# Performance work log

Hardware: AMD Instinct MI355X
Metric: run time of the kernel (lower is better)

The kernel has to match this reference:

```python
import jax, jax.numpy as jnp
from jax import lax
import numpy as np

SEQ_LEN = 96; PRED_LEN = 96; SIGNAL_LEN = 16; NUM_NODES = 256
EMBED = 128; HIDDEN = 64; K_NN = 8; S_SCALE = 2.0; CHEB_ORDER = 2
MA_K = 3; BATCH = 16
C_FREQ = SIGNAL_LEN // 2 + 1          # 9 rfft bins
M_NODES = NUM_NODES * C_FREQ          # nodes per sample graph


def _sin_posemb(pos, dim):
    half = dim // 2
    freqs = 1.0 / (10000.0 ** (np.arange(half) / half))
    ang = pos[:, None] * freqs[None, :]
    return np.concatenate([np.sin(ang), np.cos(ang)], axis=-1).astype(np.float32)


def setup_inputs():
    key = jax.random.key(0)
    ks = jax.random.split(key, 12)
    x = jax.random.normal(ks[0], (BATCH, SEQ_LEN, NUM_NODES), jnp.float32)
    # Chebyshev (order 2) approx of Haar framelet filters cos(xi/2), sin(xi/2) on [0, pi]
    t = np.linspace(-1.0, 1.0, 201); xi = (t + 1.0) * np.pi / 2.0
    ch = np.polynomial.chebyshev
    approx = np.stack([ch.chebfit(t, np.cos(xi / 2.0), CHEB_ORDER),
                       ch.chebfit(t, np.sin(xi / 2.0), CHEB_ORDER)]).astype(np.float32)
    freq_emb = _sin_posemb(np.arange(C_FREQ, dtype=np.float32) * S_SCALE, EMBED)
    sc = (2.0 / EMBED) ** 0.5
    return dict(
        x=x,
        approx=jnp.asarray(approx),                 # [F=2, K=3]
        theta=jnp.ones((2,), jnp.float32),
        fr_Wr=jax.random.normal(ks[1], (EMBED, EMBED), jnp.float32) * sc,
        fr_Wi=jax.random.normal(ks[2], (EMBED, EMBED), jnp.float32) * sc,
        eo_Wr=jax.random.normal(ks[3], (1, EMBED), jnp.float32) * sc,
        eo_Wi=jax.random.normal(ks[4], (1, EMBED), jnp.float32) * sc,
        freq_emb=jnp.asarray(freq_emb),             # [C, EMBED]
        n1_w=jnp.ones((NUM_NODES,), jnp.float32), n1_b=jnp.zeros((NUM_NODES,), jnp.float32),
        n2_w=jnp.ones((NUM_NODES,), jnp.float32), n2_b=jnp.zeros((NUM_NODES,), jnp.float32),
        W1_w=jax.random.normal(ks[5], (HIDDEN, SEQ_LEN), jnp.float32) * (1.0 / SEQ_LEN ** 0.5),
        W1_b=jnp.zeros((HIDDEN,), jnp.float32),
        W2_w=jax.random.normal(ks[6], (HIDDEN, HIDDEN), jnp.float32) * (1.0 / HIDDEN ** 0.5),
        W2_b=jnp.zeros((HIDDEN,), jnp.float32),
        Wt_w=jax.random.normal(ks[7], (HIDDEN, SEQ_LEN), jnp.float32) * (1.0 / SEQ_LEN ** 0.5),
        Wt_b=jnp.zeros((HIDDEN,), jnp.float32),
        W3_w=jax.random.normal(ks[8], (PRED_LEN, HIDDEN), jnp.float32) * (1.0 / HIDDEN ** 0.5),
        W3_b=jnp.zeros((PRED_LEN,), jnp.float32),
    )


def _clinear(z, Wr, Wi):
    xr, xi = z.real, z.imag
    return lax.complex(xr @ Wr.T - xi @ Wi.T, xr @ Wi.T + xi @ Wr.T)


def _csilu(z):
    return lax.complex(jax.nn.silu(z.real), jax.nn.silu(z.imag))


def _cheb_prop(h, row, col, ew, coeffs):
    # Chebyshev recurrence with A_norm(h) = scatter_add(row, (ew/s) * h[col])
    w = (ew / S_SCALE)[:, None]
    def A(hh):
        return jnp.zeros_like(hh).at[row].add(w * hh[col])
    Tx0 = h
    out = coeffs[0] * Tx0
    Tx1 = -A(Tx0)
    out = out + coeffs[1] * Tx1
    for ki in range(2, CHEB_ORDER + 1):
        Tx2 = -2.0 * A(Tx1) - Tx0
        out = out + coeffs[ki] * Tx2
        Tx0, Tx1 = Tx1, Tx2
    return out


def _knn_one(feat):
    # feat [M, 2] -> symmetrised degree-normalised KNN edges
    sq = jnp.sum(feat * feat, axis=1)
    d2 = sq[:, None] + sq[None, :] - 2.0 * (feat @ feat.T)
    d2 = jnp.where(jnp.eye(M_NODES, dtype=bool), jnp.inf, d2)
    idx = lax.top_k(-d2, K_NN)[1]                      # smallest distances
    src = jnp.repeat(jnp.arange(M_NODES), K_NN)
    dst = idx.reshape(-1)
    r = jnp.concatenate([src, dst])
    c = jnp.concatenate([dst, src])
    deg = jnp.zeros((M_NODES,), jnp.float32).at[r].add(1.0)
    dinv = (deg + 1e-8) ** -0.5
    return r, c, dinv[r] * dinv[c]


def _moving_avg(x):
    pad = MA_K // 2
    front = jnp.repeat(x[:, :1, :], pad, axis=1)
    back = jnp.repeat(x[:, -1:, :], MA_K - 1 - pad, axis=1)
    xp = jnp.concatenate([front, x, back], axis=1)     # (B, T+k-1, N)
    cs = jnp.cumsum(xp, axis=1)
    cs = jnp.concatenate([jnp.zeros_like(cs[:, :1, :]), cs], axis=1)
    return (cs[:, MA_K:, :] - cs[:, :-MA_K, :]) / MA_K  # (B, T, N)


def _inorm(h, w, b):
    mu = jnp.mean(h, axis=-1, keepdims=True)
    var = jnp.mean((h - mu) ** 2, axis=-1, keepdims=True)
    return (h - mu) / jnp.sqrt(var + 1e-5) * w[None, :, None] + b[None, :, None]


def _forward(x, approx, theta, fr_Wr, fr_Wi, eo_Wr, eo_Wi, freq_emb,
             n1_w, n1_b, n2_w, n2_b, W1_w, W1_b, W2_w, W2_b, Wt_w, Wt_b, W3_w, W3_b):
    B, T, N = x.shape
    trend = _moving_avg(x)
    seasonal = x - trend
    S = jnp.fft.rfft(seasonal, n=SIGNAL_LEN, axis=1, norm='ortho')   # (B, C, N) c64
    S_perm = jnp.transpose(S, (0, 2, 1))                             # (B, N, C)
    node_feat = S_perm[..., None] * freq_emb                         # (B, N, C, E) c64
    batch_x = node_feat.reshape(B * M_NODES, EMBED)
    sg = S_perm.reshape(B, M_NODES)
    feat = lax.stop_gradient(jnp.stack([sg.real, sg.imag], axis=-1))  # (B, M, 2)
    rs, cs_, ews = jax.vmap(_knn_one)(feat)
    off = (jnp.arange(B) * M_NODES)[:, None]
    row = (rs + off).reshape(-1)
    col = (cs_ + off).reshape(-1)
    ew = ews.reshape(-1)
    # framelet layer: sum of F filtered Chebyshev propagations
    acc = jnp.zeros_like(batch_x)
    for i in range(approx.shape[0]):
        acc = acc + theta[i] * _cheb_prop(batch_x, row, col, ew, approx[i])
    h = _csilu(_clinear(acc, fr_Wr, fr_Wi))
    S_out = _clinear(h, eo_Wr, eo_Wi).reshape(B, N, C_FREQ)
    H = jnp.fft.irfft(jnp.transpose(S_out, (0, 2, 1)), n=SEQ_LEN, axis=1, norm='ortho')
    H = jnp.transpose(H, (0, 2, 1))                                  # (B, N, T)
    H = jax.nn.silu(_inorm(H, n1_w, n1_b))
    H = H @ W1_w.T + W1_b
    H = jax.nn.silu(_inorm(H, n2_w, n2_b))
    H = H @ W2_w.T + W2_b
    trend_emb = jnp.transpose(trend, (0, 2, 1)) @ Wt_w.T + Wt_b
    return (H + trend_emb) @ W3_w.T + W3_b                           # (B, N, pred_len)


def reference(x, approx, theta, fr_Wr, fr_Wi, eo_Wr, eo_Wi, freq_emb,
              n1_w, n1_b, n2_w, n2_b, W1_w, W1_b, W2_w, W2_b, Wt_w, Wt_b, W3_w, W3_b):
    return _forward(x, approx, theta, fr_Wr, fr_Wi, eo_Wr, eo_Wi, freq_emb,
                    n1_w, n1_b, n2_w, n2_b, W1_w, W1_b, W2_w, W2_b, Wt_w, Wt_b, W3_w, W3_b)
```

## Files before the change

### kernel.cpp

```cpp
#include <hip/hip_runtime.h>
#include <math.h>
#include <float.h>

#define BATCH 16
#define SEQ 96
#define NNODE 256
#define CFREQ 9
#define MNODE (NNODE * CFREQ)
#define BM (BATCH * MNODE)
#define KNN 8
#define EMBED 128
#define HIDDEN 64
#define TN (SEQ * NNODE)
#define KCAP 64
#define NBLK (BM / 256)
#define HROWS 16
#define FEW (CFREQ * EMBED)

__constant__ float COS16[16] = {
    1.0f, 0.9238795325112867f, 0.7071067811865476f, 0.3826834323650898f,
    0.0f, -0.3826834323650898f, -0.7071067811865476f, -0.9238795325112867f,
    -1.0f, -0.9238795325112867f, -0.7071067811865476f, -0.3826834323650898f,
    0.0f, 0.3826834323650898f, 0.7071067811865476f, 0.9238795325112867f};
__constant__ float SIN16[16] = {
    0.0f, 0.3826834323650898f, 0.7071067811865476f, 0.9238795325112867f,
    1.0f, 0.9238795325112867f, 0.7071067811865476f, 0.3826834323650898f,
    0.0f, -0.3826834323650898f, -0.7071067811865476f, -0.9238795325112867f,
    -1.0f, -0.9238795325112867f, -0.7071067811865476f, -0.3826834323650898f};

static __device__ __forceinline__ float silu_f(float x) {
    return x / (1.0f + expf(-x));
}

static __device__ __forceinline__ float rank_h(float2 fj, float xi2, float yi2) {
    float sqj = __fmaf_rn(fj.y, fj.y, __fmul_rn(fj.x, fj.x));
    return __fmaf_rn(xi2, fj.x, __fmaf_rn(yi2, fj.y, sqj));
}

__global__ void __launch_bounds__(256) prep_kernel(
    const float* __restrict__ x, float* __restrict__ S, int* __restrict__ cnt,
    const float* __restrict__ femb, const float* __restrict__ Wr,
    const float* __restrict__ Wi, float* __restrict__ FE, int* __restrict__ gtotal) {
    int gid = blockIdx.x * 256 + threadIdx.x;
    if (gid < BM) {
        if (gid == 0) *gtotal = 0;
        cnt[gid] = 0;
        int b = gid / MNODE;
        int m = gid - b * MNODE;
        int n = m / CFREQ;
        int c = m - n * CFREQ;
        const float* xb = x + b * TN + n;
        float xv[17];
        #pragma unroll
        for (int t = 0; t < 17; ++t) xv[t] = xb[t * NNODE];
        float re = 0.0f, im = 0.0f;
        #pragma unroll
        for (int t = 0; t < 16; ++t) {
            int tm = t > 0 ? t - 1 : 0;
            float tr = (xv[tm] + xv[t] + xv[t + 1]) * (1.0f / 3.0f);
            float s = xv[t] - tr;
            int k = (c * t) & 15;
            re += s * COS16[k];
            im -= s * SIN16[k];
        }
        S[gid * 2 + 0] = re * 0.25f;
        S[gid * 2 + 1] = im * 0.25f;
    } else {
        int f = gid - BM;
        if (f < FEW) {
            int c = f / EMBED;
            int e = f - c * EMBED;
            float ar = 0.0f, ai = 0.0f;
            for (int k = 0; k < EMBED; ++k) {
                float fv = femb[c * EMBED + k];
                ar += fv * Wr[e * EMBED + k];
                ai += fv * Wi[e * EMBED + k];
            }
            FE[f * 2 + 0] = ar;
            FE[f * 2 + 1] = ai;
        }
    }
}

__global__ void __launch_bounds__(256, 8) knn_kernel(const float* __restrict__ S,
                                                     int* __restrict__ idx, int* __restrict__ cnt) {
    __shared__ float2 f[MNODE];
    __shared__ unsigned long long kbuf[4][KCAP];
    int b = blockIdx.y;
    int tid = threadIdx.x;
    for (int t = tid; t < MNODE; t += 256) {
        f[t] = make_float2(S[(b * MNODE + t) * 2 + 0], S[(b * MNODE + t) * 2 + 1]);
    }
    __syncthreads();
    int wave = tid >> 6, lane = tid & 63;
    int i = blockIdx.x * 4 + wave;
    float2 fi = f[i];
    float xi2 = __fmul_rn(-2.0f, fi.x), yi2 = __fmul_rn(-2.0f, fi.y);
    int lane_i = __builtin_amdgcn_readfirstlane(i & 63);
    int k_i    = __builtin_amdgcn_readfirstlane(i >> 6);

    float h[36];
    float mymin = FLT_MAX;
    #pragma unroll
    for (int k = 0; k < 36; ++k) {
        int j = lane + (k << 6);
        float hh = rank_h(f[j], xi2, yi2);
        if (k == k_i && lane == lane_i) hh = FLT_MAX;
        h[k] = hh;
        mymin = fminf(mymin, hh);
    }
    float g = mymin;
    g = fminf(g, __shfl_xor(g, 1, 64));
    g = fminf(g, __shfl_xor(g, 2, 64));
    g = fminf(g, __shfl_xor(g, 4, 64));
    float T = g;
    T = fmaxf(T, __shfl_xor(T, 8, 64));
    T = fmaxf(T, __shfl_xor(T, 16, 64));
    T = fmaxf(T, __shfl_xor(T, 32, 64));
    unsigned long long* mybuf = kbuf[wave];
    const unsigned long long lmask = (1ull << lane) - 1ull;
    int total = 0;
    #pragma unroll
    for (int k = 0; k < 36; ++k) {
        bool pred = h[k] <= T;
        unsigned long long mask = __ballot(pred);
        if (pred) {
            int pos = total + (int)__popcll(mask & lmask);
            if (pos < KCAP) {
                unsigned int bits = __float_as_uint(h[k]);
                if (bits == 0x80000000u) bits = 0u;
                unsigned int s = bits ^ (unsigned int)(((int)bits >> 31) | 0x80000000);
                mybuf[pos] = ((unsigned long long)s << 32) | (unsigned int)(lane + (k << 6));
            }
        }
        total += (int)__popcll(mask);
    }

    if (total >= KNN && total <= KCAP) {
        int padded = (total + 7) & ~7;
        if (lane < padded - total) mybuf[total + lane] = ~0ull;
        for (int p = lane; p < total; p += 64) {
            unsigned long long mykey = mybuf[p];
            int rank = 0;
            for (int q = 0; q < padded; q += 8) {
                const ulonglong2* bp = (const ulonglong2*)&mybuf[q];
                ulonglong2 a = bp[0], b2 = bp[1], c2 = bp[2], d2 = bp[3];
                rank += (int)(a.x  < mykey) + (int)(a.y  < mykey)
                      + (int)(b2.x < mykey) + (int)(b2.y < mykey)
                      + (int)(c2.x < mykey) + (int)(c2.y < mykey)
                      + (int)(d2.x < mykey) + (int)(d2.y < mykey);
            }
            if (rank < KNN) {
                int j = (int)(unsigned int)(mykey & 0xFFFFFFFFull);
                idx[(b * MNODE + i) * KNN + rank] = j;
                atomicAdd(&cnt[b * MNODE + j], 1);
            }
        }
    } else {
        const unsigned long long SENT = ~0ull;
        unsigned long long k0 = SENT, k1 = SENT, k2 = SENT, k3 = SENT,
                           k4 = SENT, k5 = SENT, k6 = SENT, k7 = SENT;
        #pragma unroll
        for (int k = 0; k < 36; ++k) {
            unsigned int bits = __float_as_uint(h[k]);
            if (bits == 0x80000000u) bits = 0u;
            unsigned int s = bits ^ (unsigned int)(((int)bits >> 31) | 0x80000000);
            unsigned long long key = ((unsigned long long)s << 32) | (unsigned int)(lane + (k << 6));
            if (key < k7) {
                k7 = key;
                if (k7 < k6) { unsigned long long t = k6; k6 = k7; k7 = t; }
                if (k6 < k5) { unsigned long long t = k5; k5 = k6; k6 = t; }
                if (k5 < k4) { unsigned long long t = k4; k4 = k5; k5 = t; }
                if (k4 < k3) { unsigned long long t = k3; k3 = k4; k4 = t; }
                if (k3 < k2) { unsigned long long t = k2; k2 = k3; k3 = t; }
                if (k2 < k1) { unsigned long long t = k1; k1 = k2; k2 = t; }
                if (k1 < k0) { unsigned long long t = k0; k0 = k1; k1 = t; }
            }
        }
        unsigned long long mywin = 0;
        #pragma unroll
        for (int r = 0; r < KNN; ++r) {
            unsigned long long hh = k0;
            #pragma unroll
            for (int off = 32; off > 0; off >>= 1) {
                unsigned long long o = __shfl_xor(hh, off, 64);
                if (o < hh) hh = o;
            }
            if (lane == r) mywin = hh;
            if (k0 == hh) {
                k0 = k1; k1 = k2; k2 = k3; k3 = k4; k4 = k5; k5 = k6; k6 = k7; k7 = SENT;
            }
        }
        if (lane < KNN) {
            int j = (int)(unsigned int)(mywin & 0xFFFFFFFFull);
            idx[(b * MNODE + i) * KNN + lane] = j;
            atomicAdd(&cnt[b * MNODE + j], 1);
        }
    }
}

__global__ void __launch_bounds__(256) scan_kernel(
    const int* __restrict__ cnt, const float* __restrict__ S,
    float* __restrict__ dinv, float* __restrict__ PS,
    int* __restrict__ gtotal, int2* __restrict__ oc, int* __restrict__ fptr) {
    __shared__ int wsum[4];
    __shared__ int sbase;
    int tid = threadIdx.x;
    int lane = tid & 63, wv = tid >> 6;
    int gid = blockIdx.x * 256 + tid;
    int v = cnt[gid];
    float deg = (float)(KNN + v);
    float dv = 1.0f / sqrtf(deg + 1e-8f);
    dinv[gid] = dv;
    PS[gid * 2 + 0] = dv * S[gid * 2 + 0];
    PS[gid * 2 + 1] = dv * S[gid * 2 + 1];
    int x = v;
    #pragma unroll
    for (int off = 1; off < 64; off <<= 1) {
        int y = __shfl_up(x, off, 64);
        if (lane >= off) x += y;
    }
    if (lane == 63) wsum[wv] = x;
    __syncthreads();
    if (tid == 0) sbase = atomicAdd(gtotal, wsum[0] + wsum[1] + wsum[2] + wsum[3]);
    __syncthreads();
    int base = sbase;
    for (int w = 0; w < wv; ++w) base += wsum[w];
    int o = base + x - v;
    oc[gid] = make_int2(o, v);
    fptr[gid] = o;
}

__global__ void fill_kernel(const int* __restrict__ idx,
                            int* __restrict__ fptr, int* __restrict__ rev) {
    int gid = blockIdx.x * blockDim.x + threadIdx.x;
    if (gid >= BM * KNN) return;
    int b = gid / (MNODE * KNN);
    int rem = gid - b * (MNODE * KNN);
    int i = rem / KNN;
    int gj = b * MNODE + idx[gid];
    int pos = atomicAdd(&fptr[gj], 1);
    rev[pos] = b * MNODE + i;
}

__global__ void __launch_bounds__(256) gather1_kernel(
    const int* __restrict__ idx, const int2* __restrict__ oc,
    const int* __restrict__ rev, const float* __restrict__ dinv, const float* __restrict__ PS,
    float* __restrict__ zA, float* __restrict__ zAw) {
    int gid = blockIdx.x * blockDim.x + threadIdx.x;
    if (gid >= BM * CFREQ) return;
    int gi = gid / CFREQ;
    int c = gid - gi * CFREQ;
    int b = gi / MNODE;
    float ax = 0.0f, ay = 0.0f;
    #pragma unroll
    for (int k = 0; k < KNN; ++k) {
        int gj = b * MNODE + idx[gi * KNN + k];
        bool m = (gj % CFREQ) == c;
        float2 p = ((const float2*)PS)[gj];
        ax += m ? p.x : 0.0f;
        ay += m ? p.y : 0.0f;
    }
    int2 ocv = oc[gi];
    int o = ocv.x, e = o + ocv.y;
    for (int p_ = o; p_ < e; ++p_) {
        int gk = rev[p_];
        bool m = (gk % CFREQ) == c;
        float2 p = ((const float2*)PS)[gk];
        ax += m ? p.x : 0.0f;
        ay += m ? p.y : 0.0f;
    }
    float dv = dinv[gi];
    float s = dv * 0.5f;
    float zx = s * ax, zy = s * ay;
    zA[gid * 2 + 0] = zx;
    zA[gid * 2 + 1] = zy;
    zAw[gid * 2 + 0] = dv * zx;
    zAw[gid * 2 + 1] = dv * zy;
}

__global__ void __launch_bounds__(256) g2proj_kernel(
    const int* __restrict__ idx, const int2* __restrict__ oc,
    const int* __restrict__ rev, const float* __restrict__ dinv,
    const float* __restrict__ zA, const float* __restrict__ zAw,
    const float* __restrict__ S, const float* __restrict__ FE,
    const float* __restrict__ eoWr, const float* __restrict__ eoWi,
    const float* __restrict__ theta, const float* __restrict__ approx,
    float* __restrict__ Sout) {
    __shared__ float2 zfb[4][CFREQ];
    int wave = threadIdx.x >> 6;
    int lane = threadIdx.x & 63;
    int r = blockIdx.x * 4 + wave;
    if (r >= BM) return;
    float a0 = theta[0] * approx[0] + theta[1] * approx[3];
    float a1 = theta[0] * approx[1] + theta[1] * approx[4];
    float a2 = theta[0] * approx[2] + theta[1] * approx[5];
    float ca = a0 - a2, cb = -a1, cc = 2.0f * a2;
    int b = r / MNODE;
    int2 ocv = oc[r];
    if (lane < 36) {
        int c = lane >> 2, sub = lane & 3;
        float ax = 0.0f, ay = 0.0f;
        #pragma unroll
        for (int k = sub; k < KNN; k += 4) {
            int gj = b * MNODE + idx[r * KNN + k];
            float2 v = ((const float2*)zAw)[gj * CFREQ + c];
            ax += v.x;
            ay += v.y;
        }
        int o = ocv.x, e = o + ocv.y;
        for (int p = o + sub; p < e; p += 4) {
            int gk = rev[p];
            float2 v = ((const float2*)zAw)[gk * CFREQ + c];
            ax += v.x;
            ay += v.y;
        }
        ax += __shfl_xor(ax, 1, 64);  ay += __shfl_xor(ay, 1, 64);
        ax += __shfl_xor(ax, 2, 64);  ay += __shfl_xor(ay, 2, 64);
        if (sub == 0) {
            float s = dinv[r] * 0.5f;
            float2 za = ((const float2*)zA)[r * CFREQ + c];
            zfb[wave][c] = make_float2(cb * za.x + cc * (s * ax),
                                       cb * za.y + cc * (s * ay));
        }
    }
    int cr = r % CFREQ;
    float sr = S[r * 2 + 0], si = S[r * 2 + 1];
    int e1 = lane + 64;
    float ur0 = 0.0f, ui0 = 0.0f, ur1 = 0.0f, ui1 = 0.0f;
    #pragma unroll
    for (int c = 0; c < CFREQ; ++c) {
        float2 zf = zfb[wave][c];
        float zr = zf.x, zi = zf.y;
        if (c == cr) { zr += ca * sr; zi += ca * si; }
        float fr0 = FE[(c * EMBED + lane) * 2 + 0], fi0 = FE[(c * EMBED + lane) * 2 + 1];
        float fr1 = FE[(c * EMBED + e1) * 2 + 0],  fi1 = FE[(c * EMBED + e1) * 2 + 1];
        ur0 += zr * fr0 - zi * fi0;  ui0 += zr * fi0 + zi * fr0;
        ur1 += zr * fr1 - zi * fi1;  ui1 += zr * fi1 + zi * fr1;
    }
    float hr0 = silu_f(ur0), hi0 = silu_f(ui0);
    float hr1 = silu_f(ur1), hi1 = silu_f(ui1);
    float wr0 = eoWr[lane], wi0 = eoWi[lane], wr1 = eoWr[e1], wi1 = eoWi[e1];
    float p = hr0 * wr0 - hi0 * wi0 + hr1 * wr1 - hi1 * wi1;
    float q = hr0 * wi0 + hi0 * wr0 + hr1 * wi1 + hi1 * wr1;
    #pragma unroll
    for (int off = 32; off > 0; off >>= 1) {
        p += __shfl_down(p, off, 64);
        q += __shfl_down(q, off, 64);
    }
    if (lane == 0) {
        Sout[r * 2 + 0] = p;
        Sout[r * 2 + 1] = q;
    }
}

__global__ void __launch_bounds__(1024) head_kernel(
    const float* __restrict__ Sout, const float* __restrict__ x,
    const float* __restrict__ n1w, const float* __restrict__ n1b,
    const float* __restrict__ n2w, const float* __restrict__ n2b,
    const float* __restrict__ W1w, const float* __restrict__ W1b,
    const float* __restrict__ W2w, const float* __restrict__ W2b,
    const float* __restrict__ Wtw, const float* __restrict__ Wtb,
    const float* __restrict__ W3w, const float* __restrict__ W3b,
    float* __restrict__ out) {
    __shared__ float tabc[96], tabs[96];
    __shared__ float srow[HROWS][18];
    __shared__ float tbuf[HROWS][96];
    __shared__ float hraw[HROWS][96];
    __shared__ float sH[HROWS][96];
    __shared__ float h2[HROWS][64];
    __shared__ float s3[HROWS][64];
    __shared__ float red[HROWS][2];
    __shared__ float wbuf[6240];
    int tid = threadIdx.x;
    int wave = tid >> 6, lane = tid & 63;
    int bn0 = blockIdx.x * HROWS;
    if (tid < 96) {
        double a = 6.283185307179586476925286766559 * (double)tid / 96.0;
        tabc[tid] = (float)cos(a);
        tabs[tid] = (float)sin(a);
    }
    for (int i = tid; i < HROWS * 96; i += 1024) {
        int g = i / 96, t = i - g * 96;
        int bn = bn0 + g;
        hraw[g][t] = x[(bn >> 8) * TN + t * NNODE + (bn & 255)];
    }
    if (tid < HROWS * 18) {
        int g = tid / 18, k = tid - g * 18;
        srow[g][k] = Sout[(bn0 + g) * 18 + k];
    }
    __syncthreads();
    for (int i = tid; i < HROWS * 96; i += 1024) {
        int g = i / 96, t = i - g * 96;
        int tm = t > 0 ? t - 1 : 0;
        int tp = t < SEQ - 1 ? t + 1 : SEQ - 1;
        tbuf[g][t] = (hraw[g][tm] + hraw[g][t] + hraw[g][tp]) * (1.0f / 3.0f);
    }
    __syncthreads();
    for (int i = tid; i < HROWS * 96; i += 1024) {
        int g = i / 96, t = i - g * 96;
        float acc = srow[g][0];
        #pragma unroll
        for (int c = 1; c < CFREQ; ++c) {
            int k = (c * t) % 96;
            acc += 2.0f * (srow[g][2 * c] * tabc[k] - srow[g][2 * c + 1] * tabs[k]);
        }
        hraw[g][t] = acc * 0.10206207261596575f;
    }
    __syncthreads();
    {
        float v = hraw[wave][lane] + ((lane < 32) ? hraw[wave][64 + lane] : 0.0f);
        #pragma unroll
        for (int off = 32; off > 0; off >>= 1) v += __shfl_down(v, off, 64);
        if (lane == 0) red[wave][0] = v * (1.0f / 96.0f);
    }
    __syncthreads();
    {
        float mu = red[wave][0];
        float d0 = hraw[wave][lane] - mu;
        float v = d0 * d0;
        if (lane < 32) { float d1 = hraw[wave][64 + lane] - mu; v += d1 * d1; }
        #pragma unroll
        for (int off = 32; off > 0; off >>= 1) v += __shfl_down(v, off, 64);
        if (lane == 0) red[wave][1] = v * (1.0f / 96.0f);
    }
    __syncthreads();
    for (int i = tid; i < HROWS * 96; i += 1024) {
        int g = i / 96, t = i - g * 96;
        int n = (bn0 + g) & 255;
        float xn = (hraw[g][t] - red[g][0]) / sqrtf(red[g][1] + 1e-5f) * n1w[n] + n1b[n];
        sH[g][t] = silu_f(xn);
    }
    for (int i = tid; i < HIDDEN * 96; i += 1024) {
        int rr = i / 96;
        wbuf[rr * 97 + (i - rr * 96)] = W1w[i];
    }
    __syncthreads();
    float v1;
    {
        float acc = W1b[lane];
        #pragma unroll 8
        for (int t = 0; t < 96; ++t) acc += sH[wave][t] * wbuf[lane * 97 + t];
        v1 = acc;
    }
    {
        float s = v1;
        #pragma unroll
        for (int off = 32; off > 0; off >>= 1) s += __shfl_down(s, off, 64);
        s = __shfl(s, 0, 64);
        float mu2 = s * (1.0f / 64.0f);
        float d = v1 - mu2;
        float vs = d * d;
        #pragma unroll
        for (int off = 32; off > 0; off >>= 1) vs += __shfl_down(vs, off, 64);
        vs = __shfl(vs, 0, 64);
        float var2 = vs * (1.0f / 64.0f);
        int n = (bn0 + wave) & 255;
        float xn = (v1 - mu2) / sqrtf(var2 + 1e-5f) * n2w[n] + n2b[n];
        h2[wave][lane] = silu_f(xn);
    }
    __syncthreads();
    for (int i = tid; i < HIDDEN * HIDDEN; i += 1024) {
        wbuf[(i >> 6) * 65 + (i & 63)] = W2w[i];
    }
    __syncthreads();
    float v3;
    {
        float acc = W2b[lane];
        #pragma unroll 8
        for (int h = 0; h < 64; ++h) acc += h2[wave][h] * wbuf[lane * 65 + h];
        v3 = acc;
    }
    __syncthreads();
    for (int i = tid; i < HIDDEN * 96; i += 1024) {
        int rr = i / 96;
        wbuf[rr * 97 + (i - rr * 96)] = Wtw[i];
    }
    __syncthreads();
    {
        float acc = Wtb[lane];
        #pragma unroll 8
        for (int t = 0; t < 96; ++t) acc += tbuf[wave][t] * wbuf[lane * 97 + t];
        s3[wave][lane] = v3 + acc;
    }
    __syncthreads();
    for (int i = tid; i < 96 * HIDDEN; i += 1024) {
        wbuf[(i >> 6) * 65 + (i & 63)] = W3w[i];
    }
    __syncthreads();
    for (int i = tid; i < HROWS * 96; i += 1024) {
        int g = i / 96, t = i - g * 96;
        float acc = W3b[t];
        #pragma unroll 8
        for (int h = 0; h < 64; ++h) acc += s3[g][h] * wbuf[t * 65 + h];
        out[(bn0 + g) * 96 + t] = acc;
    }
}

extern "C" void kernel_launch(void* const* d_in, const int* in_sizes, int n_in,
                              void* d_out, int out_size, void* d_ws, size_t ws_size,
                              hipStream_t stream) {
    const float* x     = (const float*)d_in[0];
    const float* approx= (const float*)d_in[1];
    const float* theta = (const float*)d_in[2];
    const float* frWr  = (const float*)d_in[3];
    const float* frWi  = (const float*)d_in[4];
    const float* eoWr  = (const float*)d_in[5];
    const float* eoWi  = (const float*)d_in[6];
    const float* femb  = (const float*)d_in[7];
    const float* n1w   = (const float*)d_in[8];
    const float* n1b   = (const float*)d_in[9];
    const float* n2w   = (const float*)d_in[10];
    const float* n2b   = (const float*)d_in[11];
    const float* W1w   = (const float*)d_in[12];
    const float* W1b   = (const float*)d_in[13];
    const float* W2w   = (const float*)d_in[14];
    const float* W2b   = (const float*)d_in[15];
    const float* Wtw   = (const float*)d_in[16];
    const float* Wtb   = (const float*)d_in[17];
    const float* W3w   = (const float*)d_in[18];
    const float* W3b   = (const float*)d_in[19];
    float* out = (float*)d_out;

    char* ws = (char*)d_ws;
    size_t off = 0;
    auto alloc = [&](size_t bytes) -> void* {
        void* p = ws + off;
        off = (off + bytes + 255) & ~(size_t)255;
        return p;
    };
    float* S     = (float*)alloc((size_t)BM * 2 * 4);
    int*   idx   = (int*)  alloc((size_t)BM * KNN * 4);
    float* dinv  = (float*)alloc((size_t)BM * 4);
    float* PS    = (float*)alloc((size_t)BM * 2 * 4);
    float* FE    = (float*)alloc((size_t)FEW * 2 * 4);
    float* Sout  = (float*)alloc((size_t)BM * 2 * 4);
    int2*  oc    = (int2*) alloc((size_t)BM * 8);
    int*   rev   = (int*)  alloc((size_t)BM * KNN * 4);
    float* zA    = (float*)alloc((size_t)BM * CFREQ * 2 * 4);
    float* zAw   = (float*)alloc((size_t)BM * CFREQ * 2 * 4);
    int*   cnt   = (int*)  alloc((size_t)BM * 4);
    int*   fptr  = (int*)  alloc((size_t)BM * 4);
    int*   gtotal= (int*)  alloc(256);

    prep_kernel<<<(BM + FEW + 255) / 256, 256, 0, stream>>>(x, S, cnt, femb, frWr, frWi, FE, gtotal);
    knn_kernel<<<dim3(MNODE / 4, BATCH), 256, 0, stream>>>(S, idx, cnt);
    scan_kernel<<<NBLK, 256, 0, stream>>>(cnt, S, dinv, PS, gtotal, oc, fptr);
    fill_kernel<<<(BM * KNN + 255) / 256, 256, 0, stream>>>(idx, fptr, rev);
    gather1_kernel<<<(BM * CFREQ + 255) / 256, 256, 0, stream>>>(idx, oc, rev, dinv, PS, zA, zAw);
    g2proj_kernel<<<BM / 4, 256, 0, stream>>>(idx, oc, rev, dinv, zA, zAw, S, FE,
                                              eoWr, eoWi, theta, approx, Sout);
    head_kernel<<<BATCH * NNODE / HROWS, 1024, 0, stream>>>(Sout, x, n1w, n1b, n2w, n2b,
                                                            W1w, W1b, W2w, W2b, Wtw, Wtb, W3w, W3b, out);
}
```

Measured before the change: 239.0 us.

## Build reverse adjacency in kNN kernel with fixed-capacity buckets, drop scan and fill

The kNN kernel now writes each reverse edge straight into a fixed-capacity per-node bucket (RCAP slots), using the atomicAdd return value as the slot. Edges past capacity go to a global overflow list. This removes the separate prefix-scan and fill kernels along with the dinv/PS buffers, and degree normalisation is recomputed from cnt on the fly in the gather kernels. In exchange the rev buffer is larger and strided, and the gathers do extra cnt lookups plus a linear overflow scan when a node has very high in-degree.

```diff
diff --git a/kernel.cpp b/kernel.cpp
--- a/kernel.cpp
+++ b/kernel.cpp
@@ -13,7 +13,7 @@
 #define HIDDEN 64
 #define TN (SEQ * NNODE)
 #define KCAP 64
-#define NBLK (BM / 256)
+#define RCAP 64
 #define HROWS 16
 #define FEW (CFREQ * EMBED)
 
@@ -32,6 +32,10 @@
     return x / (1.0f + expf(-x));
 }
 
+static __device__ __forceinline__ float dinv_of(int c) {
+    return 1.0f / sqrtf((float)(KNN + c) + 1e-8f);
+}
+
 static __device__ __forceinline__ float rank_h(float2 fj, float xi2, float yi2) {
     float sqj = __fmaf_rn(fj.y, fj.y, __fmul_rn(fj.x, fj.x));
     return __fmaf_rn(xi2, fj.x, __fmaf_rn(yi2, fj.y, sqj));
@@ -40,10 +44,10 @@
 __global__ void __launch_bounds__(256) prep_kernel(
     const float* __restrict__ x, float* __restrict__ S, int* __restrict__ cnt,
     const float* __restrict__ femb, const float* __restrict__ Wr,
-    const float* __restrict__ Wi, float* __restrict__ FE, int* __restrict__ gtotal) {
+    const float* __restrict__ Wi, float* __restrict__ FE, int* __restrict__ ovfcnt) {
     int gid = blockIdx.x * 256 + threadIdx.x;
     if (gid < BM) {
-        if (gid == 0) *gtotal = 0;
+        if (gid == 0) *ovfcnt = 0;
         cnt[gid] = 0;
         int b = gid / MNODE;
         int m = gid - b * MNODE;
@@ -82,8 +86,9 @@
     }
 }
 
-__global__ void __launch_bounds__(256, 8) knn_kernel(const float* __restrict__ S,
-                                                     int* __restrict__ idx, int* __restrict__ cnt) {
+__global__ void __launch_bounds__(256, 8) knn_kernel(
+    const float* __restrict__ S, int* __restrict__ idx, int* __restrict__ cnt,
+    int* __restrict__ rev, int2* __restrict__ ovf, int* __restrict__ ovfcnt) {
     __shared__ float2 f[MNODE];
     __shared__ unsigned long long kbuf[4][KCAP];
     int b = blockIdx.y;
@@ -136,6 +141,7 @@
         total += (int)__popcll(mask);
     }
 
+    int gi = b * MNODE + i;
     if (total >= KNN && total <= KCAP) {
         int padded = (total + 7) & ~7;
         if (lane < padded - total) mybuf[total + lane] = ~0ull;
@@ -152,8 +158,15 @@
             }
             if (rank < KNN) {
                 int j = (int)(unsigned int)(mykey & 0xFFFFFFFFull);
-                idx[(b * MNODE + i) * KNN + rank] = j;
-                atomicAdd(&cnt[b * MNODE + j], 1);
+                int gj = b * MNODE + j;
+                idx[gi * KNN + rank] = j;
+                int pos = atomicAdd(&cnt[gj], 1);
+                if (pos < RCAP) {
+                    rev[gj * RCAP + pos] = gi;
+                } else {
+                    int t = atomicAdd(ovfcnt, 1);
+                    ovf[t] = make_int2(gj, gi);
+                }
             }
         }
     } else {
@@ -193,59 +206,23 @@
         }
         if (lane < KNN) {
             int j = (int)(unsigned int)(mywin & 0xFFFFFFFFull);
-            idx[(b * MNODE + i) * KNN + lane] = j;
-            atomicAdd(&cnt[b * MNODE + j], 1);
-        }
-    }
-}
-
-__global__ void __launch_bounds__(256) scan_kernel(
-    const int* __restrict__ cnt, const float* __restrict__ S,
-    float* __restrict__ dinv, float* __restrict__ PS,
-    int* __restrict__ gtotal, int2* __restrict__ oc, int* __restrict__ fptr) {
-    __shared__ int wsum[4];
-    __shared__ int sbase;
-    int tid = threadIdx.x;
-    int lane = tid & 63, wv = tid >> 6;
-    int gid = blockIdx.x * 256 + tid;
-    int v = cnt[gid];
-    float deg = (float)(KNN + v);
-    float dv = 1.0f / sqrtf(deg + 1e-8f);
-    dinv[gid] = dv;
-    PS[gid * 2 + 0] = dv * S[gid * 2 + 0];
-    PS[gid * 2 + 1] = dv * S[gid * 2 + 1];
-    int x = v;
-    #pragma unroll
-    for (int off = 1; off < 64; off <<= 1) {
-        int y = __shfl_up(x, off, 64);
-        if (lane >= off) x += y;
-    }
-    if (lane == 63) wsum[wv] = x;
-    __syncthreads();
-    if (tid == 0) sbase = atomicAdd(gtotal, wsum[0] + wsum[1] + wsum[2] + wsum[3]);
-    __syncthreads();
-    int base = sbase;
-    for (int w = 0; w < wv; ++w) base += wsum[w];
-    int o = base + x - v;
-    oc[gid] = make_int2(o, v);
-    fptr[gid] = o;
-}
-
-__global__ void fill_kernel(const int* __restrict__ idx,
-                            int* __restrict__ fptr, int* __restrict__ rev) {
-    int gid = blockIdx.x * blockDim.x + threadIdx.x;
-    if (gid >= BM * KNN) return;
-    int b = gid / (MNODE * KNN);
-    int rem = gid - b * (MNODE * KNN);
-    int i = rem / KNN;
-    int gj = b * MNODE + idx[gid];
-    int pos = atomicAdd(&fptr[gj], 1);
-    rev[pos] = b * MNODE + i;
+            int gj = b * MNODE + j;
+            idx[gi * KNN + lane] = j;
+            int pos = atomicAdd(&cnt[gj], 1);
+            if (pos < RCAP) {
+                rev[gj * RCAP + pos] = gi;
+            } else {
+                int t = atomicAdd(ovfcnt, 1);
+                ovf[t] = make_int2(gj, gi);
+            }
+        }
+    }
 }
 
 __global__ void __launch_bounds__(256) gather1_kernel(
-    const int* __restrict__ idx, const int2* __restrict__ oc,
-    const int* __restrict__ rev, const float* __restrict__ dinv, const float* __restrict__ PS,
+    const int* __restrict__ idx, const int* __restrict__ cnt,
+    const int* __restrict__ rev, const int2* __restrict__ ovf,
+    const int* __restrict__ ovfcnt, const float* __restrict__ S,
     float* __restrict__ zA, float* __restrict__ zAw) {
     int gid = blockIdx.x * blockDim.x + threadIdx.x;
     if (gid >= BM * CFREQ) return;
@@ -257,20 +234,36 @@
     for (int k = 0; k < KNN; ++k) {
         int gj = b * MNODE + idx[gi * KNN + k];
         bool m = (gj % CFREQ) == c;
-        float2 p = ((const float2*)PS)[gj];
-        ax += m ? p.x : 0.0f;
-        ay += m ? p.y : 0.0f;
-    }
-    int2 ocv = oc[gi];
-    int o = ocv.x, e = o + ocv.y;
-    for (int p_ = o; p_ < e; ++p_) {
-        int gk = rev[p_];
+        float dvj = dinv_of(cnt[gj]);
+        float2 p = ((const float2*)S)[gj];
+        ax += m ? dvj * p.x : 0.0f;
+        ay += m ? dvj * p.y : 0.0f;
+    }
+    int cn = cnt[gi];
+    int e = cn < RCAP ? cn : RCAP;
+    for (int p_ = 0; p_ < e; ++p_) {
+        int gk = rev[gi * RCAP + p_];
         bool m = (gk % CFREQ) == c;
-        float2 p = ((const float2*)PS)[gk];
-        ax += m ? p.x : 0.0f;
-        ay += m ? p.y : 0.0f;
-    }
-    float dv = dinv[gi];
+        float dvk = dinv_of(cnt[gk]);
+        float2 p = ((const float2*)S)[gk];
+        ax += m ? dvk * p.x : 0.0f;
+        ay += m ? dvk * p.y : 0.0f;
+    }
+    if (cn > RCAP) {
+        int tot = *ovfcnt;
+        for (int t = 0; t < tot; ++t) {
+            int2 o = ovf[t];
+            if (o.x == gi) {
+                int gk = o.y;
+                bool m = (gk % CFREQ) == c;
+                float dvk = dinv_of(cnt[gk]);
+                float2 p = ((const float2*)S)[gk];
+                ax += m ? dvk * p.x : 0.0f;
+                ay += m ? dvk * p.y : 0.0f;
+            }
+        }
+    }
+    float dv = dinv_of(cn);
     float s = dv * 0.5f;
     float zx = s * ax, zy = s * ay;
     zA[gid * 2 + 0] = zx;
@@ -280,8 +273,9 @@
 }
 
 __global__ void __launch_bounds__(256) g2proj_kernel(
-    const int* __restrict__ idx, const int2* __restrict__ oc,
-    const int* __restrict__ rev, const float* __restrict__ dinv,
+    const int* __restrict__ idx, const int* __restrict__ cnt,
+    const int* __restrict__ rev, const int2* __restrict__ ovf,
+    const int* __restrict__ ovfcnt,
     const float* __restrict__ zA, const float* __restrict__ zAw,
     const float* __restrict__ S, const float* __restrict__ FE,
     const float* __restrict__ eoWr, const float* __restrict__ eoWi,
@@ -297,7 +291,7 @@
     float a2 = theta[0] * approx[2] + theta[1] * approx[5];
     float ca = a0 - a2, cb = -a1, cc = 2.0f * a2;
     int b = r / MNODE;
-    int2 ocv = oc[r];
+    int cn = cnt[r];
     if (lane < 36) {
         int c = lane >> 2, sub = lane & 3;
         float ax = 0.0f, ay = 0.0f;
@@ -308,17 +302,28 @@
             ax += v.x;
             ay += v.y;
         }
-        int o = ocv.x, e = o + ocv.y;
-        for (int p = o + sub; p < e; p += 4) {
-            int gk = rev[p];
+        int e = cn < RCAP ? cn : RCAP;
+        for (int p = sub; p < e; p += 4) {
+            int gk = rev[r * RCAP + p];
             float2 v = ((const float2*)zAw)[gk * CFREQ + c];
             ax += v.x;
             ay += v.y;
         }
+        if (cn > RCAP) {
+            int tot = *ovfcnt;
+            for (int t = sub; t < tot; t += 4) {
+                int2 o = ovf[t];
+                if (o.x == r) {
+                    float2 v = ((const float2*)zAw)[o.y * CFREQ + c];
+                    ax += v.x;
+                    ay += v.y;
+                }
+            }
+        }
         ax += __shfl_xor(ax, 1, 64);  ay += __shfl_xor(ay, 1, 64);
         ax += __shfl_xor(ax, 2, 64);  ay += __shfl_xor(ay, 2, 64);
         if (sub == 0) {
-            float s = dinv[r] * 0.5f;
+            float s = dinv_of(cn) * 0.5f;
             float2 za = ((const float2*)zA)[r * CFREQ + c];
             zfb[wave][c] = make_float2(cb * za.x + cc * (s * ax),
                                        cb * za.y + cc * (s * ay));
@@ -531,24 +536,19 @@
     };
     float* S     = (float*)alloc((size_t)BM * 2 * 4);
     int*   idx   = (int*)  alloc((size_t)BM * KNN * 4);
-    float* dinv  = (float*)alloc((size_t)BM * 4);
-    float* PS    = (float*)alloc((size_t)BM * 2 * 4);
     float* FE    = (float*)alloc((size_t)FEW * 2 * 4);
     float* Sout  = (float*)alloc((size_t)BM * 2 * 4);
-    int2*  oc    = (int2*) alloc((size_t)BM * 8);
-    int*   rev   = (int*)  alloc((size_t)BM * KNN * 4);
+    int*   rev   = (int*)  alloc((size_t)BM * RCAP * 4);
     float* zA    = (float*)alloc((size_t)BM * CFREQ * 2 * 4);
     float* zAw   = (float*)alloc((size_t)BM * CFREQ * 2 * 4);
     int*   cnt   = (int*)  alloc((size_t)BM * 4);
-    int*   fptr  = (int*)  alloc((size_t)BM * 4);
-    int*   gtotal= (int*)  alloc(256);
-
-    prep_kernel<<<(BM + FEW + 255) / 256, 256, 0, stream>>>(x, S, cnt, femb, frWr, frWi, FE, gtotal);
-    knn_kernel<<<dim3(MNODE / 4, BATCH), 256, 0, stream>>>(S, idx, cnt);
-    scan_kernel<<<NBLK, 256, 0, stream>>>(cnt, S, dinv, PS, gtotal, oc, fptr);
-    fill_kernel<<<(BM * KNN + 255) / 256, 256, 0, stream>>>(idx, fptr, rev);
-    gather1_kernel<<<(BM * CFREQ + 255) / 256, 256, 0, stream>>>(idx, oc, rev, dinv, PS, zA, zAw);
-    g2proj_kernel<<<BM / 4, 256, 0, stream>>>(idx, oc, rev, dinv, zA, zAw, S, FE,
+    int2*  ovf   = (int2*) alloc((size_t)BM * KNN * 8);
+    int*   ovfcnt= (int*)  alloc(256);
+
+    prep_kernel<<<(BM + FEW + 255) / 256, 256, 0, stream>>>(x, S, cnt, femb, frWr, frWi, FE, ovfcnt);
+    knn_kernel<<<dim3(MNODE / 4, BATCH), 256, 0, stream>>>(S, idx, cnt, rev, ovf, ovfcnt);
+    gather1_kernel<<<(BM * CFREQ + 255) / 256, 256, 0, stream>>>(idx, cnt, rev, ovf, ovfcnt, S, zA, zAw);
+    g2proj_kernel<<<BM / 4, 256, 0, stream>>>(idx, cnt, rev, ovf, ovfcnt, zA, zAw, S, FE,
                                               eoWr, eoWi, theta, approx, Sout);
     head_kernel<<<BATCH * NNODE / HROWS, 1024, 0, stream>>>(Sout, x, n1w, n1b, n2w, n2b,
                                                             W1w, W1b, W2w, W2b, Wtw, Wtb, W3w, W3b, out);
```

Result: faster. 225.0 us, median of 2 (-5.8%).
